# Optimization experiments

Measured on AMD Instinct MI355X. Metric: run time of the kernel, lower is better.

Reference implementation:

```python
import jax, jax.numpy as jnp
import numpy as np


def _patchify(x, p):
    # x: [B, V, H, W] -> [B, V, L, p*p] with L = (H/p)*(W/p), matching Conv2d(kernel=stride=p)
    B, V, H, W = x.shape
    hp, wp = H // p, W // p
    x = x.reshape(B, V, hp, p, wp, p)
    x = x.transpose(0, 1, 2, 4, 3, 5)  # [B, V, hp, wp, p, p]
    return x.reshape(B, V, hp * wp, p * p)


def setup_inputs() -> dict:
    key = jax.random.key(0)
    ks = jax.random.split(key, 12)
    B, V, H, W, p, D = 2, 16, 128, 256, 4, 1024
    L = (H // p) * (W // p)  # 2048
    std = 0.02
    return {
        "x": jax.random.normal(ks[0], (B, V, H, W), jnp.float32),
        "proj_w": jax.random.normal(ks[1], (V, D, p * p), jnp.float32) * std,
        "proj_b": jnp.zeros((V, D), jnp.float32),
        "channel_embed": jax.random.normal(ks[2], (1, V, D), jnp.float32) * std,
        "pos_embed": jax.random.normal(ks[3], (1, L, D), jnp.float32) * std,
        "channel_query": jax.random.normal(ks[4], (1, 1, D), jnp.float32) * std,
        "wq": jax.random.normal(ks[5], (D, D), jnp.float32) * std,
        "wk": jax.random.normal(ks[6], (D, D), jnp.float32) * std,
        "wv": jax.random.normal(ks[7], (D, D), jnp.float32) * std,
        "bq": jnp.zeros((D,), jnp.float32),
        "bk": jnp.zeros((D,), jnp.float32),
        "bv": jnp.zeros((D,), jnp.float32),
        "wo": jax.random.normal(ks[8], (D, D), jnp.float32) * std,
        "bo": jnp.zeros((D,), jnp.float32),
        "num_heads": 16,
    }


def reference(x, proj_w, proj_b, channel_embed, pos_embed, channel_query,
              wq, wk, wv, bq, bk, bv, wo, bo, num_heads):
    D = proj_w.shape[1]
    p = int(round(np.sqrt(proj_w.shape[-1])))
    nh = int(num_heads)
    dh = D // nh

    # per-variable patch embed (Conv2d k=stride=p == patch-matmul)
    patches = _patchify(x, p)                                   # [B, V, L, p*p]
    tok = jnp.einsum('bvlk,vdk->bvld', patches, proj_w)         # [B, V, L, D]
    tok = tok + proj_b[None, :, None, :]

    # add variable (channel) and positional embeddings
    tok = tok + channel_embed[:, :, None, :] + pos_embed[:, None, :, :]

    # aggregate_variables: single-query MHA over V, batched over B*L
    h = tok.transpose(0, 2, 1, 3)                               # [B, L, V, D]
    q = channel_query[0, 0] @ wq.T + bq                         # [D]
    qh = q.reshape(nh, dh)
    k = (jnp.einsum('blvd,ed->blve', h, wk) + bk).reshape(*h.shape[:3], nh, dh)
    v = (jnp.einsum('blvd,ed->blve', h, wv) + bv).reshape(*h.shape[:3], nh, dh)
    scores = jnp.einsum('he,blvhe->blhv', qh, k) / np.sqrt(dh)  # [B, L, nh, V]
    attn = jax.nn.softmax(scores, axis=-1)
    ctx = jnp.einsum('blhv,blvhe->blhe', attn, v)               # [B, L, nh, dh]
    ctx = ctx.reshape(h.shape[0], h.shape[1], D)
    out = ctx @ wo.T + bo                                       # [B, L, D]
    return out
```

## Files before the change

### kernel.cpp

```cpp
#include <hip/hip_runtime.h>
#include <hip/hip_bf16.h>

using bf16 = __hip_bfloat16;
using bf16x8 = __attribute__((ext_vector_type(8))) short;
using f32x4  = __attribute__((ext_vector_type(4))) float;

__device__ inline unsigned short f2bu(float f){ bf16 h = __float2bfloat16(f); return *(unsigned short*)&h; }
__device__ inline void async_cp16(const void* g, void* l){
  __builtin_amdgcn_global_load_lds((const __attribute__((address_space(1))) void*)g,
                                   (__attribute__((address_space(3))) void*)l, 16, 0, 0);
}
union BF8 { unsigned short s[8]; bf16x8 v; };

constexpr int D_ = 1024, L_ = 2048;
constexpr int CN = 384;

__device__ inline size_t w3idx(int row, int col){
  const int hh = row >> 6, m = row & 15, dt = (row >> 4) & 3;
  const int vp = col >> 5, quad = (col >> 3) & 3, j = col & 7;
  return (size_t)hh*18432 + vp*2048 + dt*512 + quad*128 + m*8 + j;
}

__global__ __launch_bounds__(256) void k_prep2(const float* __restrict__ wv, const float* __restrict__ wo,
                                               const float* __restrict__ pe,
                                               const float* __restrict__ proj_w, const float* __restrict__ proj_b,
                                               const float* __restrict__ ce, const float* __restrict__ cq,
                                               const float* __restrict__ wq, const float* __restrict__ bq,
                                               const float* __restrict__ wk,
                                               unsigned short* __restrict__ Ab, unsigned short* __restrict__ wo_b,
                                               unsigned short* __restrict__ pe_b,
                                               unsigned short* __restrict__ Btb){
  __shared__ float t[64][17];
  __shared__ float qL[64];
  const int blk = blockIdx.x;
  const int tid = threadIdx.x;
  if (blk < 4096){
    int i = blk*256 + tid;
    const float* src; unsigned short* dst; size_t off;
    if (i < 262144){ src = wv; dst = Ab;   off = i; }
    else if (i < 524288){ src = wo; dst = wo_b; off = i - 262144; }
    else           { src = pe; dst = pe_b; off = i - 524288; }
    float4 v = *(const float4*)(src + off*4);
    *(ushort4*)(dst + off*4) = make_ushort4(f2bu(v.x), f2bu(v.y), f2bu(v.z), f2bu(v.w));
  } else if (blk < 4352){
    const int r_ = blk - 4096;
    const int v = r_ >> 4, dd0 = (r_ & 15)*64;
    { const int r = tid >> 2, kq = tid & 3;
      float4 a = *(const float4*)(proj_w + ((size_t)(v*D_ + dd0 + r))*16 + kq*4);
      t[r][kq*4+0]=a.x; t[r][kq*4+1]=a.y; t[r][kq*4+2]=a.z; t[r][kq*4+3]=a.w; }
    __syncthreads();
    { const int k = tid >> 4, c0 = (tid & 15)*4;
      ushort4 o = make_ushort4(f2bu(t[c0+0][k]), f2bu(t[c0+1][k]), f2bu(t[c0+2][k]), f2bu(t[c0+3][k]));
      *(ushort4*)(Btb + (size_t)(v*16+k)*D_ + dd0 + c0) = o; }
    if (tid < 16){
      const int c0 = tid*4;
      float4 pb = *(const float4*)(proj_b + v*D_ + dd0 + c0);
      float4 cc = *(const float4*)(ce     + v*D_ + dd0 + c0);
      ushort4 o = make_ushort4(f2bu(pb.x+cc.x), f2bu(pb.y+cc.y), f2bu(pb.z+cc.z), f2bu(pb.w+cc.w));
      *(ushort4*)(Btb + (size_t)(256+v)*D_ + dd0 + c0) = o;
    }
  } else {
    const int hh = blk - 4352;
    const int wave = tid >> 6, lane = tid & 63;
    {
      float cqv[16];
      #pragma unroll
      for (int k=0;k<16;++k) cqv[k] = cq[lane + 64*k];
      #pragma unroll
      for (int j=0;j<16;++j){
        const int e = hh*64 + wave*16 + j;
        const float* wr = wq + (size_t)e*D_;
        float p = 0.f;
        #pragma unroll
        for (int k=0;k<16;++k) p += cqv[k]*wr[lane + 64*k];
        #pragma unroll
        for (int m=32;m>=1;m>>=1) p += __shfl_xor(p, m, 64);
        if (lane==0) qL[wave*16+j] = p + bq[e];
      }
    }
    __syncthreads();
    #pragma unroll
    for (int dd=0; dd<4; ++dd){
      const int d = dd*256 + tid;
      float s0=0.f, s1=0.f, s2=0.f, s3=0.f;
      #pragma unroll
      for (int j=0;j<16;++j) s0 += qL[j]    * wk[(size_t)(hh*64      + j)*D_ + d];
      #pragma unroll
      for (int j=0;j<16;++j) s1 += qL[16+j] * wk[(size_t)(hh*64 + 16 + j)*D_ + d];
      #pragma unroll
      for (int j=0;j<16;++j) s2 += qL[32+j] * wk[(size_t)(hh*64 + 32 + j)*D_ + d];
      #pragma unroll
      for (int j=0;j<16;++j) s3 += qL[48+j] * wk[(size_t)(hh*64 + 48 + j)*D_ + d];
      Ab[(size_t)(1024+hh)*D_ + d] = f2bu(((s0+s1)+(s2+s3))*0.125f);
    }
  }
}

template<int MFRAG, bool BIAS, bool WB2>
__device__ inline void gemm_body(unsigned short* As, unsigned short* Bs,
                                 const unsigned short* __restrict__ Abf, const unsigned short* __restrict__ Bt,
                                 const float* __restrict__ bias, float* __restrict__ C,
                                 unsigned short* __restrict__ W, const float* __restrict__ bvp,
                                 int m0, int n0, int K, int ldc, int Mvalid){
  const int tid = threadIdx.x;
  const int wave = tid >> 6, lane = tid & 63;
  const int wm = wave & 1, wn = wave >> 1;
  const int lm = lane & 15, kg4 = lane >> 4;
  f32x4 acc[MFRAG][4];
  #pragma unroll
  for (int mf=0;mf<MFRAG;++mf)
    #pragma unroll
    for (int nf=0;nf<4;++nf) acc[mf][nf] = (f32x4){0.f,0.f,0.f,0.f};
  for (int k0=0; k0<K; k0+=128){
    #pragma unroll
    for (int i=0;i<2*MFRAG;++i){
      int idx = i*256 + tid;
      int row = idx >> 4, g = (idx & 15) ^ (row & 7);
      async_cp16(Abf + (size_t)(m0+row)*K + k0 + g*8, &As[idx*8]);
    }
    #pragma unroll
    for (int i=0;i<8;++i){
      int idx = i*256 + tid;
      int row = idx >> 4, g = (idx & 15) ^ (row & 7);
      async_cp16(Bt + (size_t)(n0+row)*K + k0 + g*8, &Bs[idx*8]);
    }
    __syncthreads();
    #pragma unroll
    for (int c=0;c<4;++c){
      bf16x8 af[MFRAG], bfr[4];
      #pragma unroll
      for (int f=0;f<MFRAG;++f){
        int row = wm*16*MFRAG + f*16 + lm;
        af[f] = *(const bf16x8*)(&As[row*128 + (((c*4+kg4) ^ (row&7)))*8]);
      }
      #pragma unroll
      for (int f=0;f<4;++f){
        int colr = wn*64 + f*16 + lm;
        bfr[f] = *(const bf16x8*)(&Bs[colr*128 + (((c*4+kg4) ^ (colr&7)))*8]);
      }
      #pragma unroll
      for (int mf=0;mf<MFRAG;++mf)
        #pragma unroll
        for (int nf=0;nf<4;++nf)
          acc[mf][nf] = __builtin_amdgcn_mfma_f32_16x16x32_bf16(af[mf], bfr[nf], acc[mf][nf], 0,0,0);
    }
    __syncthreads();
  }
  #pragma unroll
  for (int nf=0;nf<4;++nf){
    int col = n0 + wn*64 + nf*16 + lm;
    float bval = BIAS ? bias[col] : 0.f;
    #pragma unroll
    for (int mf=0;mf<MFRAG;++mf){
      #pragma unroll
      for (int r=0;r<4;++r){
        int row = m0 + wm*16*MFRAG + mf*16 + kg4*4 + r;
        if (row < Mvalid){
          float v = acc[mf][nf][r];
          C[(size_t)row*ldc + col] = v + bval;
          if (WB2 && row < 1024){
            if (col < 256)      W[w3idx(row,col)] = f2bu(v);
            else if (col < 272) W[w3idx(row,col)] = f2bu(v + bvp[row]);
            else if (col < 288) W[w3idx(row,col)] = 0;
          }
        }
      }
    }
  }
}

__global__ __launch_bounds__(256) void k_gemmCP2(const unsigned short* __restrict__ Ab,
                                                 const unsigned short* __restrict__ Btb,
                                                 const unsigned short* __restrict__ pe_b,
                                                 const float* __restrict__ bv,
                                                 float* __restrict__ Cbig, unsigned short* __restrict__ Wb2,
                                                 float* __restrict__ P2){
  __shared__ unsigned short As[64*128];
  __shared__ unsigned short Bs[128*128];
  if (blockIdx.x < 51){
    int bx = blockIdx.x % 3, by = blockIdx.x / 3;
    gemm_body<2,false,true>(As, Bs, Ab, Btb, nullptr, Cbig, Wb2, bv, by*64, bx*128, 1024, CN, 1040);
  } else {
    int b = blockIdx.x - 51;
    int bx = b >> 6, by = b & 63;
    gemm_body<1,false,false>(As, Bs, pe_b, Ab, nullptr, P2, nullptr, nullptr, by*32, bx*128, 1024, 1024, 2048);
  }
}

__global__ __launch_bounds__(256) void k_gemmOut(const unsigned short* __restrict__ ctxF,
                                                 const unsigned short* __restrict__ wo_b,
                                                 const float* __restrict__ bo, float* __restrict__ C){
  __shared__ unsigned short As[64*128];
  __shared__ unsigned short Bs[128*128];
  gemm_body<2,true,false>(As, Bs, ctxF, wo_b, bo, C, nullptr, nullptr,
                          blockIdx.x*64, blockIdx.y*128, 1024, 1024, 4096);
}

__global__ __launch_bounds__(1024) void k_fused10(const float* __restrict__ x,
                                                  const float* __restrict__ Cbig,
                                                  const unsigned short* __restrict__ W3,
                                                  const float* __restrict__ P2,
                                                  unsigned short* __restrict__ ctxF){
  __shared__ float patchP[16*260];
  __shared__ float attnT[16*320];
  __shared__ __align__(16) unsigned short S[16*1032];
  const int tid = threadIdx.x;
  const int bb  = blockIdx.x >> 7;
  const int sg  = blockIdx.x & 127;
  unsigned short* ctx = ctxF + (size_t)bb*L_*D_;
  const int l0 = sg*16;
  {
    const int u = tid & 15, pi = (tid >> 4) & 3, v = tid >> 6;
    const int hi = l0 >> 6, wi0 = l0 & 63;
    const float* xp = x + ((size_t)((bb*16+v)*128 + hi*4 + pi)*256 + (wi0+u)*4);
    float4 r = *(const float4*)xp;
    float* dst = &patchP[u*260 + v*16 + pi*4];
    dst[0]=r.x; dst[1]=r.y; dst[2]=r.z; dst[3]=r.w;
  }
  __syncthreads();
  if (tid < 256){
    const int s = tid >> 4, h = tid & 15;
    const float* qrow = Cbig + (size_t)(1024+h)*CN;
    const float* prow = &patchP[s*260];
    float4 qc0 = *(const float4*)(qrow+256);
    float4 qc1 = *(const float4*)(qrow+260);
    float4 qc2 = *(const float4*)(qrow+264);
    float4 qc3 = *(const float4*)(qrow+268);
    float qcv[16] = {qc0.x,qc0.y,qc0.z,qc0.w, qc1.x,qc1.y,qc1.z,qc1.w,
                     qc2.x,qc2.y,qc2.z,qc2.w, qc3.x,qc3.y,qc3.z,qc3.w};
    float sc[16];
    #pragma unroll
    for (int v=0; v<16; ++v){
      const float* qp = qrow + v*16;
      const float* pp = prow + v*16;
      float4 qa = *(const float4*)(qp+0),  qb = *(const float4*)(qp+4);
      float4 qc = *(const float4*)(qp+8),  qd = *(const float4*)(qp+12);
      float4 pa = *(const float4*)(pp+0),  pb2 = *(const float4*)(pp+4);
      float4 pc = *(const float4*)(pp+8),  pd = *(const float4*)(pp+12);
      float a = qcv[v];
      a += qa.x*pa.x + qa.y*pa.y + qa.z*pa.z + qa.w*pa.w;
      a += qb.x*pb2.x + qb.y*pb2.y + qb.z*pb2.z + qb.w*pb2.w;
      a += qc.x*pc.x + qc.y*pc.y + qc.z*pc.z + qc.w*pc.w;
      a += qd.x*pd.x + qd.y*pd.y + qd.z*pd.z + qd.w*pd.w;
      sc[v] = a;
    }
    float mx = sc[0];
    #pragma unroll
    for (int v=1;v<16;++v) mx = fmaxf(mx, sc[v]);
    float sum = 0.f;
    #pragma unroll
    for (int v=0;v<16;++v){ sc[v] = __expf(sc[v]-mx); sum += sc[v]; }
    float inv = 1.f/sum;
    float* arow = &attnT[h*320 + s*20];
    #pragma unroll
    for (int v=0;v<16;++v) arow[v] = sc[v]*inv;
  }
  __syncthreads();
  const int wave = tid >> 6, lane = tid & 63;
  const int m = lane & 15, quad = lane >> 4;
  const int hh = wave;
  const float* at = &attnT[hh*320];
  const unsigned short* wbase = W3 + (size_t)hh*18432 + lane*8;
  f32x4 acc[4];
  #pragma unroll
  for (int dt=0;dt<4;++dt) acc[dt] = (f32x4){0.f,0.f,0.f,0.f};
  #pragma unroll
  for (int vp=0; vp<9; ++vp){
    BF8 af;
    if (vp < 8){
      const int v = vp*2 + (quad>>1);
      const int k8 = (quad&1)*8;
      const float aw = at[m*20 + v];
      const float* pp = &patchP[m*260 + v*16 + k8];
      float4 p0 = *(const float4*)(pp+0);
      float4 p1 = *(const float4*)(pp+4);
      af.s[0]=f2bu(aw*p0.x); af.s[1]=f2bu(aw*p0.y); af.s[2]=f2bu(aw*p0.z); af.s[3]=f2bu(aw*p0.w);
      af.s[4]=f2bu(aw*p1.x); af.s[5]=f2bu(aw*p1.y); af.s[6]=f2bu(aw*p1.z); af.s[7]=f2bu(aw*p1.w);
    } else {
      #pragma unroll
      for (int j=0;j<8;++j)
        af.s[j] = (quad < 2) ? f2bu(at[m*20 + quad*8 + j]) : (unsigned short)0;
    }
    #pragma unroll
    for (int dt=0; dt<4; ++dt){
      const bf16x8 bf = *(const bf16x8*)(wbase + vp*2048 + dt*512);
      acc[dt] = __builtin_amdgcn_mfma_f32_16x16x32_bf16(af.v, bf, acc[dt], 0,0,0);
    }
  }
  #pragma unroll
  for (int dt=0; dt<4; ++dt){
    const int d = hh*64 + dt*16 + m;
    #pragma unroll
    for (int r=0;r<4;++r){
      const int s = quad*4 + r;
      S[s*1032 + d] = f2bu(acc[dt][r] + P2[(size_t)(l0+s)*D_ + d]);
    }
  }
  __syncthreads();
  {
    const int row = tid >> 6, ch = tid & 63;
    const unsigned short* srcp = &S[row*1032 + ch*16];
    unsigned short* dstp = ctx + (size_t)(l0+row)*D_ + ch*16;
    *(uint4*)(dstp)   = *(const uint4*)(srcp);
    *(uint4*)(dstp+8) = *(const uint4*)(srcp+8);
  }
}

extern "C" void kernel_launch(void* const* d_in, const int* in_sizes, int n_in,
                              void* d_out, int out_size, void* d_ws, size_t ws_size,
                              hipStream_t stream){
  const float* x      = (const float*)d_in[0];
  const float* proj_w = (const float*)d_in[1];
  const float* proj_b = (const float*)d_in[2];
  const float* ce     = (const float*)d_in[3];
  const float* pe     = (const float*)d_in[4];
  const float* cq     = (const float*)d_in[5];
  const float* wq     = (const float*)d_in[6];
  const float* wk     = (const float*)d_in[7];
  const float* wv     = (const float*)d_in[8];
  const float* bq     = (const float*)d_in[9];
  const float* bv     = (const float*)d_in[11];
  const float* wo     = (const float*)d_in[12];
  const float* bo     = (const float*)d_in[13];
  float* out = (float*)d_out;

  char* base = (char*)d_ws;
  unsigned short* Ab   = (unsigned short*)(base);
  unsigned short* Btb  = (unsigned short*)(base + 2359296);
  float*          Cbig = (float*)(base + 3145728);
  unsigned short* wo_b = (unsigned short*)(base + 4743168);
  unsigned short* Wb2  = (unsigned short*)(base + 6840320);
  float*          P2   = (float*)(base + 7430144);
  unsigned short* ctxF = (unsigned short*)(base + 15818752);
  unsigned short* pe_b = (unsigned short*)(base + 24207360);

  k_prep2<<<4368, 256, 0, stream>>>(wv, wo, pe, proj_w, proj_b, ce, cq, wq, bq, wk, Ab, wo_b, pe_b, Btb);
  k_gemmCP2<<<563, 256, 0, stream>>>(Ab, Btb, pe_b, bv, Cbig, Wb2, P2);
  k_fused10<<<256, 1024, 0, stream>>>(x, Cbig, Wb2, P2, ctxF);
  k_gemmOut<<<dim3(64,8), 256, 0, stream>>>(ctxF, wo_b, bo, out);
}
```

Baseline: 168.7 us.

## Fuse output projection GEMM into fused attention kernel with pre-swizzled Wo

Removes the separate k_gemmOut launch and the ctxF round trip through global memory. The fused kernel now multiplies its 16-row bf16 context tile in LDS directly against a pre-swizzled bf16 Wo using MFMA, then writes fp32 output with bias. Wo is rearranged during prep into an MFMA-fragment-friendly layout. The risk is that each of only 256 blocks now streams the full 2MB Wo for just 16 rows, so Wo traffic is high and the work per block is long and sequential.

```diff
diff --git a/kernel.cpp b/kernel.cpp
--- a/kernel.cpp
+++ b/kernel.cpp
@@ -19,6 +19,9 @@
   const int hh = row >> 6, m = row & 15, dt = (row >> 4) & 3;
   const int vp = col >> 5, quad = (col >> 3) & 3, j = col & 7;
   return (size_t)hh*18432 + vp*2048 + dt*512 + quad*128 + m*8 + j;
+}
+__device__ inline size_t wo4idx(int e, int d){
+  return ((size_t)(e>>4)<<14) + ((size_t)(d>>5)<<9) + (((d>>3)&3)<<7) + ((e&15)<<3) + (d&7);
 }
 
 __global__ __launch_bounds__(256) void k_prep2(const float* __restrict__ wv, const float* __restrict__ wo,
@@ -27,7 +30,7 @@
                                                const float* __restrict__ ce, const float* __restrict__ cq,
                                                const float* __restrict__ wq, const float* __restrict__ bq,
                                                const float* __restrict__ wk,
-                                               unsigned short* __restrict__ Ab, unsigned short* __restrict__ wo_b,
+                                               unsigned short* __restrict__ Ab, unsigned short* __restrict__ wo4,
                                                unsigned short* __restrict__ pe_b,
                                                unsigned short* __restrict__ Btb){
   __shared__ float t[64][17];
@@ -36,12 +39,19 @@
   const int tid = threadIdx.x;
   if (blk < 4096){
     int i = blk*256 + tid;
-    const float* src; unsigned short* dst; size_t off;
-    if (i < 262144){ src = wv; dst = Ab;   off = i; }
-    else if (i < 524288){ src = wo; dst = wo_b; off = i - 262144; }
-    else           { src = pe; dst = pe_b; off = i - 524288; }
-    float4 v = *(const float4*)(src + off*4);
-    *(ushort4*)(dst + off*4) = make_ushort4(f2bu(v.x), f2bu(v.y), f2bu(v.z), f2bu(v.w));
+    if (i < 262144){
+      float4 v = *(const float4*)(wv + (size_t)i*4);
+      *(ushort4*)(Ab + (size_t)i*4) = make_ushort4(f2bu(v.x), f2bu(v.y), f2bu(v.z), f2bu(v.w));
+    } else if (i < 524288){
+      size_t off = i - 262144;
+      int q = (int)(off*4); int e = q >> 10, d = q & 1023;
+      float4 v = *(const float4*)(wo + (size_t)off*4);
+      *(ushort4*)(wo4 + wo4idx(e, d)) = make_ushort4(f2bu(v.x), f2bu(v.y), f2bu(v.z), f2bu(v.w));
+    } else {
+      size_t off = i - 524288;
+      float4 v = *(const float4*)(pe + off*4);
+      *(ushort4*)(pe_b + off*4) = make_ushort4(f2bu(v.x), f2bu(v.y), f2bu(v.z), f2bu(v.w));
+    }
   } else if (blk < 4352){
     const int r_ = blk - 4096;
     const int v = r_ >> 4, dd0 = (r_ & 15)*64;
@@ -187,27 +197,19 @@
   }
 }
 
-__global__ __launch_bounds__(256) void k_gemmOut(const unsigned short* __restrict__ ctxF,
-                                                 const unsigned short* __restrict__ wo_b,
-                                                 const float* __restrict__ bo, float* __restrict__ C){
-  __shared__ unsigned short As[64*128];
-  __shared__ unsigned short Bs[128*128];
-  gemm_body<2,true,false>(As, Bs, ctxF, wo_b, bo, C, nullptr, nullptr,
-                          blockIdx.x*64, blockIdx.y*128, 1024, 1024, 4096);
-}
-
-__global__ __launch_bounds__(1024) void k_fused10(const float* __restrict__ x,
+__global__ __launch_bounds__(1024) void k_fused11(const float* __restrict__ x,
                                                   const float* __restrict__ Cbig,
                                                   const unsigned short* __restrict__ W3,
                                                   const float* __restrict__ P2,
-                                                  unsigned short* __restrict__ ctxF){
+                                                  const unsigned short* __restrict__ wo4,
+                                                  const float* __restrict__ bo,
+                                                  float* __restrict__ out){
   __shared__ float patchP[16*260];
   __shared__ float attnT[16*320];
   __shared__ __align__(16) unsigned short S[16*1032];
   const int tid = threadIdx.x;
   const int bb  = blockIdx.x >> 7;
   const int sg  = blockIdx.x & 127;
-  unsigned short* ctx = ctxF + (size_t)bb*L_*D_;
   const int l0 = sg*16;
   {
     const int u = tid & 15, pi = (tid >> 4) & 3, v = tid >> 6;
@@ -258,51 +260,75 @@
   __syncthreads();
   const int wave = tid >> 6, lane = tid & 63;
   const int m = lane & 15, quad = lane >> 4;
-  const int hh = wave;
-  const float* at = &attnT[hh*320];
-  const unsigned short* wbase = W3 + (size_t)hh*18432 + lane*8;
-  f32x4 acc[4];
-  #pragma unroll
-  for (int dt=0;dt<4;++dt) acc[dt] = (f32x4){0.f,0.f,0.f,0.f};
-  #pragma unroll
-  for (int vp=0; vp<9; ++vp){
-    BF8 af;
-    if (vp < 8){
-      const int v = vp*2 + (quad>>1);
-      const int k8 = (quad&1)*8;
-      const float aw = at[m*20 + v];
-      const float* pp = &patchP[m*260 + v*16 + k8];
-      float4 p0 = *(const float4*)(pp+0);
-      float4 p1 = *(const float4*)(pp+4);
-      af.s[0]=f2bu(aw*p0.x); af.s[1]=f2bu(aw*p0.y); af.s[2]=f2bu(aw*p0.z); af.s[3]=f2bu(aw*p0.w);
-      af.s[4]=f2bu(aw*p1.x); af.s[5]=f2bu(aw*p1.y); af.s[6]=f2bu(aw*p1.z); af.s[7]=f2bu(aw*p1.w);
-    } else {
-      #pragma unroll
-      for (int j=0;j<8;++j)
-        af.s[j] = (quad < 2) ? f2bu(at[m*20 + quad*8 + j]) : (unsigned short)0;
+  {
+    const int hh = wave;
+    const float* at = &attnT[hh*320];
+    const unsigned short* wbase = W3 + (size_t)hh*18432 + lane*8;
+    f32x4 acc[4];
+    #pragma unroll
+    for (int dt=0;dt<4;++dt) acc[dt] = (f32x4){0.f,0.f,0.f,0.f};
+    #pragma unroll
+    for (int vp=0; vp<9; ++vp){
+      BF8 af;
+      if (vp < 8){
+        const int v = vp*2 + (quad>>1);
+        const int k8 = (quad&1)*8;
+        const float aw = at[m*20 + v];
+        const float* pp = &patchP[m*260 + v*16 + k8];
+        float4 p0 = *(const float4*)(pp+0);
+        float4 p1 = *(const float4*)(pp+4);
+        af.s[0]=f2bu(aw*p0.x); af.s[1]=f2bu(aw*p0.y); af.s[2]=f2bu(aw*p0.z); af.s[3]=f2bu(aw*p0.w);
+        af.s[4]=f2bu(aw*p1.x); af.s[5]=f2bu(aw*p1.y); af.s[6]=f2bu(aw*p1.z); af.s[7]=f2bu(aw*p1.w);
+      } else {
+        #pragma unroll
+        for (int j=0;j<8;++j)
+          af.s[j] = (quad < 2) ? f2bu(at[m*20 + quad*8 + j]) : (unsigned short)0;
+      }
+      #pragma unroll
+      for (int dt=0; dt<4; ++dt){
+        const bf16x8 bf = *(const bf16x8*)(wbase + vp*2048 + dt*512);
+        acc[dt] = __builtin_amdgcn_mfma_f32_16x16x32_bf16(af.v, bf, acc[dt], 0,0,0);
+      }
     }
     #pragma unroll
     for (int dt=0; dt<4; ++dt){
-      const bf16x8 bf = *(const bf16x8*)(wbase + vp*2048 + dt*512);
-      acc[dt] = __builtin_amdgcn_mfma_f32_16x16x32_bf16(af.v, bf, acc[dt], 0,0,0);
-    }
-  }
-  #pragma unroll
-  for (int dt=0; dt<4; ++dt){
-    const int d = hh*64 + dt*16 + m;
-    #pragma unroll
-    for (int r=0;r<4;++r){
-      const int s = quad*4 + r;
-      S[s*1032 + d] = f2bu(acc[dt][r] + P2[(size_t)(l0+s)*D_ + d]);
+      const int d = hh*64 + dt*16 + m;
+      #pragma unroll
+      for (int r=0;r<4;++r){
+        const int s = quad*4 + r;
+        S[s*1032 + d] = f2bu(acc[dt][r] + P2[(size_t)(l0+s)*D_ + d]);
+      }
     }
   }
   __syncthreads();
   {
-    const int row = tid >> 6, ch = tid & 63;
-    const unsigned short* srcp = &S[row*1032 + ch*16];
-    unsigned short* dstp = ctx + (size_t)(l0+row)*D_ + ch*16;
-    *(uint4*)(dstp)   = *(const uint4*)(srcp);
-    *(uint4*)(dstp+8) = *(const uint4*)(srcp+8);
+    const int w = wave;
+    const int lm = m, kg4 = quad;
+    #pragma unroll
+    for (int pass=0; pass<2; ++pass){
+      f32x4 oacc[2];
+      oacc[0] = (f32x4){0.f,0.f,0.f,0.f};
+      oacc[1] = (f32x4){0.f,0.f,0.f,0.f};
+      for (int c=0; c<32; ++c){
+        const bf16x8 a8 = *(const bf16x8*)(&S[lm*1032 + (c*4+kg4)*8]);
+        #pragma unroll
+        for (int nf=0; nf<2; ++nf){
+          const int colgrp = (w<<2) + pass*2 + nf;
+          const bf16x8 b8 = *(const bf16x8*)(wo4 + ((size_t)colgrp<<14) + (c<<9) + lane*8);
+          oacc[nf] = __builtin_amdgcn_mfma_f32_16x16x32_bf16(a8, b8, oacc[nf], 0,0,0);
+        }
+      }
+      #pragma unroll
+      for (int nf=0; nf<2; ++nf){
+        const int col = w*64 + (pass*2+nf)*16 + lm;
+        const float bval = bo[col];
+        #pragma unroll
+        for (int r=0;r<4;++r){
+          const int row = l0 + kg4*4 + r;
+          out[(size_t)(bb*L_ + row)*D_ + col] = oacc[nf][r] + bval;
+        }
+      }
+    }
   }
 }
 
@@ -328,14 +354,12 @@
   unsigned short* Ab   = (unsigned short*)(base);
   unsigned short* Btb  = (unsigned short*)(base + 2359296);
   float*          Cbig = (float*)(base + 3145728);
-  unsigned short* wo_b = (unsigned short*)(base + 4743168);
+  unsigned short* wo4  = (unsigned short*)(base + 4743168);
   unsigned short* Wb2  = (unsigned short*)(base + 6840320);
   float*          P2   = (float*)(base + 7430144);
-  unsigned short* ctxF = (unsigned short*)(base + 15818752);
-  unsigned short* pe_b = (unsigned short*)(base + 24207360);
-
-  k_prep2<<<4368, 256, 0, stream>>>(wv, wo, pe, proj_w, proj_b, ce, cq, wq, bq, wk, Ab, wo_b, pe_b, Btb);
+  unsigned short* pe_b = (unsigned short*)(base + 15818752);
+
+  k_prep2<<<4368, 256, 0, stream>>>(wv, wo, pe, proj_w, proj_b, ce, cq, wq, bq, wk, Ab, wo4, pe_b, Btb);
   k_gemmCP2<<<563, 256, 0, stream>>>(Ab, Btb, pe_b, bv, Cbig, Wb2, P2);
-  k_fused10<<<256, 1024, 0, stream>>>(x, Cbig, Wb2, P2, ctxF);
-  k_gemmOut<<<dim3(64,8), 256, 0, stream>>>(ctxF, wo_b, bo, out);
-}
+  k_fused11<<<256, 1024, 0, stream>>>(x, Cbig, Wb2, P2, wo4, bo, out);
+}
```

Measured after the change: 171.9 us. About the same (+1.9%).
